# Kernel optimization log

Measured on AMD Instinct MI355X. Metric: run time of the kernel, lower is better.

## Reference

```python
import jax, jax.numpy as jnp
import numpy as np

IMAGE_SIZE = 224  # self.image_size; dims are all equal to this so postprocess is one bilinear resize
EPS = 1e-12      # F.normalize default eps


def setup_inputs() -> dict:
    key = jax.random.key(0)
    k1, k2 = jax.random.split(key)
    embeddings = jax.random.normal(k1, (2, 9, 256, 48, 48), dtype=jnp.float32)
    # binary class masks in {0,1}; channel 0 (background) is recomputed inside forward
    prompt_masks = jax.random.randint(k2, (2, 8, 4, 48, 48), 0, 2).astype(jnp.float32)
    dims = jnp.full((2, 1, 2), IMAGE_SIZE, dtype=jnp.int32)  # all original sizes == image_size
    return {"embeddings": embeddings, "prompt_masks": prompt_masks, "dims": dims}


def reference(embeddings, prompt_masks, dims):
    B, M, D, H, W = embeddings.shape
    HW = H * W
    q = embeddings[:, 0]            # (B, D, H, W)  query
    s = embeddings[:, 1:]           # (B, M-1, D, H, W)  supports
    # F.normalize: x / max(||x||, eps) along the feature dim
    qn = q / jnp.maximum(jnp.sqrt(jnp.sum(q * q, axis=1, keepdims=True)), EPS)
    sn = s / jnp.maximum(jnp.sqrt(jnp.sum(s * s, axis=2, keepdims=True)), EPS)

    q2 = qn.reshape(B, D, HW).transpose(0, 2, 1)              # (B, Q, D)
    s2 = sn.reshape(B, M - 1, D, HW).transpose(0, 1, 3, 2)    # (B, M1, K, D)
    sim = jnp.einsum('bqd,bmkd->bqmk', q2, s2)                # (B, Q, M1, K) cosine sims

    # nearest-resize of prompt masks to compare_size==(H,W) is identity here (same size)
    N = prompt_masks.shape[2]
    pm = prompt_masks.reshape(B, M - 1, N, HW)
    background = (pm[:, :, 1:, :].sum(axis=2) == 0).astype(sim.dtype)  # (B, M1, HW)
    pm = pm.at[:, :, 0, :].set(background)

    neg_inf = jnp.array(-jnp.inf, sim.dtype)
    logits = []
    for n in range(N):  # small fixed class count
        cm = pm[:, :, n, :][:, None]                 # (B, 1, M1, K) broadcast over Q
        masked = jnp.where(cm == 0, neg_inf, sim)    # (B, Q, M1, K)
        logits.append(masked.reshape(B, HW, -1).max(axis=-1))  # (B, Q)
    logits = jnp.stack(logits, axis=1).reshape(B, N, H, W)

    # postprocess_masks: bilinear to image_size; all original sizes == image_size so the
    # per-image second interpolate is identity and padding amounts are zero.
    out = jax.image.resize(logits, (B, N, IMAGE_SIZE, IMAGE_SIZE), method='bilinear')
    # masks[:,0][masks[:,0]==-inf] = 0  (no-op here, kept for faithfulness)
    out = out.at[:, 0].set(jnp.where(jnp.isneginf(out[:, 0]), 0.0, out[:, 0]))
    return out
```

## Files before the change

### kernel.cpp

```cpp
#include <hip/hip_runtime.h>
#include <hip/hip_bf16.h>
#include <math.h>

#define BB 2
#define MM 9
#define MS 8
#define DD 256
#define HW 2304
#define NCLS 4
#define OUTR 224

typedef float floatx4 __attribute__((ext_vector_type(4)));
typedef __bf16 bf16x8 __attribute__((ext_vector_type(8)));
typedef unsigned short ushortx8 __attribute__((ext_vector_type(8)));

__device__ __forceinline__ unsigned enc_f(float f) {
    unsigned u = __float_as_uint(f);
    return (u & 0x80000000u) ? ~u : (u | 0x80000000u);
}
__device__ __forceinline__ float dec_f(unsigned k) {
    unsigned u = (k & 0x80000000u) ? (k & 0x7FFFFFFFu) : ~k;
    return __uint_as_float(u);
}

__global__ __launch_bounds__(256) void knorm(const float* __restrict__ emb,
                                             __hip_bfloat16* __restrict__ outp,
                                             unsigned* __restrict__ enc_logits) {
    __shared__ float tile[256][33];
    __shared__ float psum[8][32];
    __shared__ float sscale[32];
    const int bm   = blockIdx.y;
    const int pix0 = blockIdx.x * 32;
    const int tid  = threadIdx.x;
    const int pc = tid & 31;
    const int dr = tid >> 5;

    int flat = (blockIdx.y * gridDim.x + blockIdx.x) * 256 + tid;
    if (flat < BB * NCLS * HW) enc_logits[flat] = 0u;

    const float* src = emb + (size_t)bm * DD * HW + pix0;
#pragma unroll
    for (int r = 0; r < 32; ++r) {
        int d = r * 8 + dr;
        tile[d][pc] = src[(size_t)d * HW + pc];
    }
    __syncthreads();
    float ss = 0.f;
#pragma unroll
    for (int s = 0; s < 32; ++s) {
        float v = tile[dr * 32 + s][pc];
        ss += v * v;
    }
    psum[dr][pc] = ss;
    __syncthreads();
    if (tid < 32) {
        float t = 0.f;
#pragma unroll
        for (int c = 0; c < 8; ++c) t += psum[c][tid];
        sscale[tid] = 1.0f / fmaxf(sqrtf(t), 1e-12f);
    }
    __syncthreads();
    __hip_bfloat16* dst = outp + (size_t)bm * HW * DD + (size_t)pix0 * DD;
#pragma unroll
    for (int r = 0; r < 32; ++r) {
        float v = tile[tid][r] * sscale[r];
        dst[(size_t)r * DD + tid] = __float2bfloat16(v);
    }
}

__device__ __forceinline__ void gld16(const unsigned short* g, unsigned short* l) {
    __builtin_amdgcn_global_load_lds((__attribute__((address_space(1))) void*)g,
                                     (__attribute__((address_space(3))) void*)l, 16, 0, 0);
}

#define BK 64
#define REDSTRIDE 132
#define SMEM_BYTES 33792

__global__ __launch_bounds__(256, 4) void kgemm(const unsigned short* __restrict__ normed,
                                                const float* __restrict__ pm,
                                                unsigned* __restrict__ enc_logits) {
    __shared__ __attribute__((aligned(16))) unsigned char smem[SMEM_BYTES];
    unsigned short* As = (unsigned short*)smem;
    unsigned short* Bs = As + 128 * 64;
    float* red = (float*)smem;

    const int ct = blockIdx.x;
    const int rt = blockIdx.y;
    const int b  = blockIdx.z;
    const int m  = ct / 18;
    const int kt = ct % 18;

    const int tid  = threadIdx.x;
    const int lane = tid & 63;
    const int wave = tid >> 6;
    const int wr = wave >> 1, wc = wave & 1;
    const int lrow = lane & 15;
    const int quad = lane >> 4;

    const unsigned short* A  = normed + (size_t)(b * MM) * (HW * DD) + (size_t)(rt * 128) * DD;
    const unsigned short* Bp = normed + (size_t)(b * MM + 1 + m) * (HW * DD) + (size_t)(kt * 128) * DD;

    const float* pmB = pm + (size_t)(b * MS + m) * NCLS * HW;
    int mj[4];
#pragma unroll
    for (int j = 0; j < 4; ++j) {
        int kp = kt * 128 + wc * 64 + j * 16 + lrow;
        float p1 = pmB[HW + kp], p2 = pmB[2 * HW + kp], p3 = pmB[3 * HW + kp];
        mj[j] = ((p1 + p2 + p3 == 0.0f) ? 1 : 0) | (p1 != 0.0f ? 2 : 0) |
                (p2 != 0.0f ? 4 : 0) | (p3 != 0.0f ? 8 : 0);
    }

    const int srq  = lane >> 3;
    const int scol = ((lane & 7) ^ srq) * 8;

    floatx4 zero = {0.f, 0.f, 0.f, 0.f};
    floatx4 acc[4][4];
#pragma unroll
    for (int i = 0; i < 4; ++i)
#pragma unroll
        for (int j = 0; j < 4; ++j) acc[i][j] = zero;

    for (int k0 = 0; k0 < DD; k0 += BK) {
#pragma unroll
        for (int q = 0; q < 4; ++q) {
            int row = wave * 32 + q * 8 + srq;
            gld16(A  + (size_t)row * DD + k0 + scol, As + (wave * 4 + q) * 512);
            gld16(Bp + (size_t)row * DD + k0 + scol, Bs + (wave * 4 + q) * 512);
        }
        __syncthreads();
#pragma unroll
        for (int kk = 0; kk < 2; ++kk) {
            bf16x8 af[4], bfr[4];
#pragma unroll
            for (int i = 0; i < 4; ++i) {
                int ar = wr * 64 + i * 16 + lrow;
                int br = wc * 64 + i * 16 + lrow;
                int pcA = (kk * 4 + quad) ^ (ar & 7);
                int pcB = (kk * 4 + quad) ^ (br & 7);
                af[i]  = __builtin_bit_cast(bf16x8, *(const ushortx8*)(As + ar * 64 + pcA * 8));
                bfr[i] = __builtin_bit_cast(bf16x8, *(const ushortx8*)(Bs + br * 64 + pcB * 8));
            }
#pragma unroll
            for (int i = 0; i < 4; ++i)
#pragma unroll
                for (int j = 0; j < 4; ++j)
                    acc[i][j] = __builtin_amdgcn_mfma_f32_16x16x32_bf16(af[i], bfr[j], acc[i][j], 0, 0, 0);
        }
        __syncthreads();
    }

    const int col32 = wc * 16 + lrow;

#pragma unroll
    for (int p = 0; p < 2; ++p) {
        if (p) __syncthreads();
        bool bit[2][4];
#pragma unroll
        for (int nn = 0; nn < 2; ++nn) {
            int n = p * 2 + nn;
#pragma unroll
            for (int j = 0; j < 4; ++j) bit[nn][j] = (mj[j] >> n) & 1;
        }
#pragma unroll
        for (int nn = 0; nn < 2; ++nn) {
#pragma unroll
            for (int i = 0; i < 4; ++i) {
                floatx4 o;
#pragma unroll
                for (int r = 0; r < 4; ++r) {
                    float t0 = bit[nn][0] ? acc[i][0][r] : -INFINITY;
                    float t1 = bit[nn][1] ? acc[i][1][r] : -INFINITY;
                    float t2 = bit[nn][2] ? acc[i][2][r] : -INFINITY;
                    float t3 = bit[nn][3] ? acc[i][3][r] : -INFINITY;
                    o[r] = fmaxf(fmaxf(t0, t1), fmaxf(t2, t3));
                }
                int rowbase = wr * 64 + i * 16 + quad * 4;
                *(floatx4*)(red + ((size_t)(nn * 32 + col32)) * REDSTRIDE + rowbase) = o;
            }
        }
        __syncthreads();
        {
            int nn  = tid >> 7;
            int row = tid & 127;
            float v = -INFINITY;
#pragma unroll
            for (int c = 0; c < 32; ++c)
                v = fmaxf(v, red[((size_t)(nn * 32 + c)) * REDSTRIDE + row]);
            int n = p * 2 + nn;
            atomicMax(enc_logits + ((size_t)b * NCLS + n) * HW + rt * 128 + row, enc_f(v));
        }
    }
}

__global__ __launch_bounds__(256) void kresize(const unsigned* __restrict__ enc_logits,
                                               float* __restrict__ out) {
    int idx = blockIdx.x * 256 + threadIdx.x;
    if (idx >= BB * NCLS * OUTR * OUTR) return;
    int ox = idx % OUTR;
    int oy = (idx / OUTR) % OUTR;
    int bn = idx / (OUTR * OUTR);
    const unsigned* src = enc_logits + (size_t)bn * HW;
    const float inv = 48.0f / 224.0f;
    float sx = (ox + 0.5f) * inv - 0.5f;
    float sy = (oy + 0.5f) * inv - 0.5f;
    int x0 = (int)floorf(sx); float fx = sx - x0;
    int y0 = (int)floorf(sy); float fy = sy - y0;
    int x0c = min(max(x0, 0), 47), x1c = min(max(x0 + 1, 0), 47);
    int y0c = min(max(y0, 0), 47), y1c = min(max(y0 + 1, 0), 47);
    float v00 = dec_f(src[y0c * 48 + x0c]), v01 = dec_f(src[y0c * 48 + x1c]);
    float v10 = dec_f(src[y1c * 48 + x0c]), v11 = dec_f(src[y1c * 48 + x1c]);
    float v = (1.f - fy) * ((1.f - fx) * v00 + fx * v01) + fy * ((1.f - fx) * v10 + fx * v11);
    if ((bn & 3) == 0 && v == -INFINITY) v = 0.f;
    out[idx] = v;
}

extern "C" void kernel_launch(void* const* d_in, const int* in_sizes, int n_in,
                              void* d_out, int out_size, void* d_ws, size_t ws_size,
                              hipStream_t stream) {
    const float* emb = (const float*)d_in[0];
    const float* pm  = (const float*)d_in[1];
    float* out = (float*)d_out;

    char* ws = (char*)d_ws;
    const size_t normed_bytes = (size_t)BB * MM * HW * DD * 2;
    __hip_bfloat16* normed = (__hip_bfloat16*)(ws);
    unsigned*       enc    = (unsigned*)(ws + normed_bytes);

    knorm<<<dim3(HW / 32, BB * MM), 256, 0, stream>>>(emb, normed, enc);
    kgemm<<<dim3(144, 18, BB), 256, 0, stream>>>((const unsigned short*)normed, pm, enc);
    kresize<<<(BB * NCLS * OUTR * OUTR + 255) / 256, 256, 0, stream>>>(enc, out);
}
```

Before: 143.1 us.

## Fuse bilinear resize into GEMM tail via atomic ticket counter; vectorize norm loads

Drops the separate resize kernel. Each GEMM block now takes a ticket from a global counter, and the last 64 blocks spin until every tile has finished, then split the bilinear upsample between them, reading the logits with agent-scope atomic loads. The norm kernel also loads input rows as float4 vectors instead of scalars. This saves a kernel launch and its gap, but the tail blocks busy-wait, and the scheme relies on all blocks making forward progress.

```diff
diff --git a/kernel.cpp b/kernel.cpp
--- a/kernel.cpp
+++ b/kernel.cpp
@@ -10,6 +10,9 @@
 #define NCLS 4
 #define OUTR 224
 
+#define TOT_TILES (144 * 18 * BB)
+#define TAIL 64
+
 typedef float floatx4 __attribute__((ext_vector_type(4)));
 typedef __bf16 bf16x8 __attribute__((ext_vector_type(8)));
 typedef unsigned short ushortx8 __attribute__((ext_vector_type(8)));
@@ -21,6 +24,9 @@
 __device__ __forceinline__ float dec_f(unsigned k) {
     unsigned u = (k & 0x80000000u) ? (k & 0x7FFFFFFFu) : ~k;
     return __uint_as_float(u);
+}
+__device__ __forceinline__ unsigned load_agent(const unsigned* p) {
+    return __hip_atomic_load(p, __ATOMIC_RELAXED, __HIP_MEMORY_SCOPE_AGENT);
 }
 
 __global__ __launch_bounds__(256) void knorm(const float* __restrict__ emb,
@@ -32,26 +38,34 @@
     const int bm   = blockIdx.y;
     const int pix0 = blockIdx.x * 32;
     const int tid  = threadIdx.x;
-    const int pc = tid & 31;
-    const int dr = tid >> 5;
 
     int flat = (blockIdx.y * gridDim.x + blockIdx.x) * 256 + tid;
-    if (flat < BB * NCLS * HW) enc_logits[flat] = 0u;
+    if (flat < BB * NCLS * HW + 1) enc_logits[flat] = 0u;
 
     const float* src = emb + (size_t)bm * DD * HW + pix0;
-#pragma unroll
-    for (int r = 0; r < 32; ++r) {
-        int d = r * 8 + dr;
-        tile[d][pc] = src[(size_t)d * HW + pc];
-    }
-    __syncthreads();
-    float ss = 0.f;
-#pragma unroll
-    for (int s = 0; s < 32; ++s) {
-        float v = tile[dr * 32 + s][pc];
-        ss += v * v;
-    }
-    psum[dr][pc] = ss;
+    {
+        const int dr = tid >> 3;
+        const int p4 = (tid & 7) * 4;
+#pragma unroll
+        for (int r = 0; r < 8; ++r) {
+            int d = r * 32 + dr;
+            floatx4 v = *(const floatx4*)(src + (size_t)d * HW + p4);
+            float* t = &tile[d][p4];
+            t[0] = v[0]; t[1] = v[1]; t[2] = v[2]; t[3] = v[3];
+        }
+    }
+    __syncthreads();
+    {
+        const int pc = tid & 31;
+        const int dr = tid >> 5;
+        float ss = 0.f;
+#pragma unroll
+        for (int s = 0; s < 32; ++s) {
+            float v = tile[dr * 32 + s][pc];
+            ss += v * v;
+        }
+        psum[dr][pc] = ss;
+    }
     __syncthreads();
     if (tid < 32) {
         float t = 0.f;
@@ -79,8 +93,11 @@
 
 __global__ __launch_bounds__(256, 4) void kgemm(const unsigned short* __restrict__ normed,
                                                 const float* __restrict__ pm,
-                                                unsigned* __restrict__ enc_logits) {
+                                                unsigned* __restrict__ enc_logits,
+                                                unsigned* __restrict__ cnt,
+                                                float* __restrict__ out) {
     __shared__ __attribute__((aligned(16))) unsigned char smem[SMEM_BYTES];
+    __shared__ int ticket_s;
     unsigned short* As = (unsigned short*)smem;
     unsigned short* Bs = As + 128 * 64;
     float* red = (float*)smem;
@@ -191,28 +208,43 @@
             atomicMax(enc_logits + ((size_t)b * NCLS + n) * HW + rt * 128 + row, enc_f(v));
         }
     }
-}
-
-__global__ __launch_bounds__(256) void kresize(const unsigned* __restrict__ enc_logits,
-                                               float* __restrict__ out) {
-    int idx = blockIdx.x * 256 + threadIdx.x;
-    if (idx >= BB * NCLS * OUTR * OUTR) return;
-    int ox = idx % OUTR;
-    int oy = (idx / OUTR) % OUTR;
-    int bn = idx / (OUTR * OUTR);
-    const unsigned* src = enc_logits + (size_t)bn * HW;
+
+    __syncthreads();
+    if (tid == 0) {
+        __threadfence();
+        ticket_s = (int)atomicAdd(cnt, 1u);
+    }
+    __syncthreads();
+    const int ticket = ticket_s;
+    if (ticket < TOT_TILES - TAIL) return;
+    if (tid == 0) {
+        while (__hip_atomic_load(cnt, __ATOMIC_ACQUIRE, __HIP_MEMORY_SCOPE_AGENT) < TOT_TILES)
+            __builtin_amdgcn_s_sleep(8);
+    }
+    __syncthreads();
+
+    const int rank = ticket - (TOT_TILES - TAIL);
+    const int chunk = (BB * NCLS * OUTR * OUTR) / TAIL;
     const float inv = 48.0f / 224.0f;
-    float sx = (ox + 0.5f) * inv - 0.5f;
-    float sy = (oy + 0.5f) * inv - 0.5f;
-    int x0 = (int)floorf(sx); float fx = sx - x0;
-    int y0 = (int)floorf(sy); float fy = sy - y0;
-    int x0c = min(max(x0, 0), 47), x1c = min(max(x0 + 1, 0), 47);
-    int y0c = min(max(y0, 0), 47), y1c = min(max(y0 + 1, 0), 47);
-    float v00 = dec_f(src[y0c * 48 + x0c]), v01 = dec_f(src[y0c * 48 + x1c]);
-    float v10 = dec_f(src[y1c * 48 + x0c]), v11 = dec_f(src[y1c * 48 + x1c]);
-    float v = (1.f - fy) * ((1.f - fx) * v00 + fx * v01) + fy * ((1.f - fx) * v10 + fx * v11);
-    if ((bn & 3) == 0 && v == -INFINITY) v = 0.f;
-    out[idx] = v;
+    for (int idx = rank * chunk + tid; idx < (rank + 1) * chunk; idx += 256) {
+        int ox = idx % OUTR;
+        int oy = (idx / OUTR) % OUTR;
+        int bn = idx / (OUTR * OUTR);
+        const unsigned* src = enc_logits + (size_t)bn * HW;
+        float sx = (ox + 0.5f) * inv - 0.5f;
+        float sy = (oy + 0.5f) * inv - 0.5f;
+        int x0 = (int)floorf(sx); float fx = sx - x0;
+        int y0 = (int)floorf(sy); float fy = sy - y0;
+        int x0c = min(max(x0, 0), 47), x1c = min(max(x0 + 1, 0), 47);
+        int y0c = min(max(y0, 0), 47), y1c = min(max(y0 + 1, 0), 47);
+        float v00 = dec_f(load_agent(src + y0c * 48 + x0c));
+        float v01 = dec_f(load_agent(src + y0c * 48 + x1c));
+        float v10 = dec_f(load_agent(src + y1c * 48 + x0c));
+        float v11 = dec_f(load_agent(src + y1c * 48 + x1c));
+        float v = (1.f - fy) * ((1.f - fx) * v00 + fx * v01) + fy * ((1.f - fx) * v10 + fx * v11);
+        if ((bn & 3) == 0 && v == -INFINITY) v = 0.f;
+        out[idx] = v;
+    }
 }
 
 extern "C" void kernel_launch(void* const* d_in, const int* in_sizes, int n_in,
@@ -226,8 +258,8 @@
     const size_t normed_bytes = (size_t)BB * MM * HW * DD * 2;
     __hip_bfloat16* normed = (__hip_bfloat16*)(ws);
     unsigned*       enc    = (unsigned*)(ws + normed_bytes);
+    unsigned*       cnt    = enc + BB * NCLS * HW;
 
     knorm<<<dim3(HW / 32, BB * MM), 256, 0, stream>>>(emb, normed, enc);
-    kgemm<<<dim3(144, 18, BB), 256, 0, stream>>>((const unsigned short*)normed, pm, enc);
-    kresize<<<(BB * NCLS * OUTR * OUTR + 255) / 256, 256, 0, stream>>>(enc, out);
-}
+    kgemm<<<dim3(144, 18, BB), 256, 0, stream>>>((const unsigned short*)normed, pm, enc, cnt, out);
+}
```

New measurement: 285.2 us. 99.3% more time.
